# Kernel tuning notes

Hardware: AMD Instinct MI355X
Metric: run time of the kernel (lower is better)

The kernel has to match this reference:

```python
import jax, jax.numpy as jnp
import numpy as np

N_NODES = 1024      # nNodes
N_EDGES = 4096      # nEdges
N_FACTORS = 64      # input feature dim (rows of kernel / paths)
BATCH = 256
NNZ_PER_ROW = 32    # nonzeros per kernel row -> iter = count_nonzero = 32 exactly
N_SOURCES = 16


def setup_inputs() -> dict:
    key = jax.random.key(0)
    k1, k2 = jax.random.split(key, 2)
    x = jax.random.normal(k1, (BATCH, N_FACTORS), dtype=jnp.float32)

    rng = np.random.default_rng(0)
    lin = rng.choice(N_NODES * N_NODES, size=N_EDGES, replace=False)
    # Edges[e] = (col, row): original scatters node_prop[i, Edges[e][1], Edges[e][0]] = paths[i][e]
    edges = np.stack([lin % N_NODES, lin // N_NODES], axis=1).astype(np.int64)

    sources = np.sort(rng.choice(N_NODES, size=N_SOURCES, replace=False)).astype(np.int64)

    # kernel ("paths") with exactly NNZ_PER_ROW nonzeros per row, so the
    # data-dependent propagation depth count_nonzero(paths[i]) == NNZ_PER_ROW
    cols = np.argsort(rng.random((N_FACTORS, N_EDGES)), axis=1)[:, :NNZ_PER_ROW]
    mask = np.zeros((N_FACTORS, N_EDGES), dtype=np.float32)
    mask[np.arange(N_FACTORS)[:, None], cols] = 1.0
    dense = np.asarray(jax.random.normal(k2, (N_FACTORS, N_EDGES), dtype=jnp.float32)) * 0.1
    kernel = jnp.asarray(dense * mask)

    return {
        "x": x,
        "kernel": kernel,
        "edges": jnp.asarray(edges),
        "sources": jnp.asarray(sources),
    }


def reference(x, kernel, edges, sources):
    F, E = kernel.shape
    N = N_NODES

    # scatter-build per-factor adjacency: node_prop[i, dst, src] = kernel[i, e]
    node_prop = jnp.zeros((F, N, N), x.dtype).at[:, edges[:, 1], edges[:, 0]].set(kernel)
    # row 0 fixed so each column sums to 1
    node_prop = node_prop.at[:, 0, :].set(1.0 - node_prop.sum(axis=1))

    source_flow = jnp.zeros((N,), x.dtype).at[sources].set(1.0)

    # data-dependent propagation depth per factor
    iters = jnp.count_nonzero(kernel, axis=1)  # [F], == NNZ_PER_ROW by construction

    # prop_flow[i] is linear in factor[i]; propagate the unit source vector per factor
    V0 = jnp.broadcast_to(source_flow, (F, N))

    def step(V, t):
        Vn = jnp.einsum('fij,fj->fi', node_prop, V)
        return jnp.where(t < iters[:, None], Vn, V), None

    V, _ = jax.lax.scan(step, V0, jnp.arange(NNZ_PER_ROW))

    # subtract factor[i] at every source node: W[i] = V[i] - 1_{sources}
    W = V - source_flow  # [F, N]

    prop_flows = x @ W        # [B, N]  (sum over factors of scaled propagated flows)
    recon = x @ kernel        # [B, E]  linear-combination reconstruction
    return prop_flows, recon
```

## Files before the change

### kernel.cpp

```cpp
#include <hip/hip_runtime.h>
#include <hip/hip_bf16.h>

#define NNODES   1024
#define NEDGES   4096
#define NFACT    64
#define NBATCH   256
#define NSRC     16
#define MAXNNZ   64
#define MAXITER  32

__global__ __launch_bounds__(64) void prop_kernel(
    const float* __restrict__ kern,
    const int*   __restrict__ edges,
    const int*   __restrict__ sources,
    float*       __restrict__ W)
{
    __shared__ float v_lds[NNODES];
    __shared__ float wbuf[MAXNNZ];
    __shared__ int   srcbuf[MAXNNZ];
    __shared__ int   dstbuf[MAXNNZ];
    __shared__ float c_lds[MAXNNZ];
    __shared__ int   cnt;

    const int f = blockIdx.x;
    const int t = threadIdx.x;

    if (t == 0) cnt = 0;
    __syncthreads();

    const float4* kern4 = (const float4*)kern;
    for (int i = 0; i < NEDGES / 4 / 64; ++i) {
        int e4 = t + i * 64;
        float4 kv = kern4[f * (NEDGES / 4) + e4];
        float vals[4] = {kv.x, kv.y, kv.z, kv.w};
        #pragma unroll
        for (int c = 0; c < 4; ++c) {
            if (vals[c] != 0.0f) {
                int e = e4 * 4 + c;
                int slot = atomicAdd(&cnt, 1);
                if (slot < MAXNNZ) {
                    wbuf[slot]   = vals[c];
                    srcbuf[slot] = edges[e * 2 + 0];
                    dstbuf[slot] = edges[e * 2 + 1];
                }
            }
        }
    }
    __syncthreads();

    int nnz = cnt;
    if (nnz > MAXNNZ) nnz = MAXNNZ;
    const int T = nnz < MAXITER ? nnz : MAXITER;

    const bool active = (t < nnz);
    const float w_e  = active ? wbuf[t]   : 0.0f;
    const int   src  = active ? srcbuf[t] : -1;
    const int   dst  = active ? dstbuf[t] : -1;

    unsigned long long gmask = 0ull;
    for (int e2 = 0; e2 < nnz; ++e2) {
        if (dstbuf[e2] == src) gmask |= (1ull << e2);
    }

    float S = (float)NSRC;
    float val = 0.0f;
    #pragma unroll
    for (int s = 0; s < NSRC; ++s) {
        if (sources[s] == src) val = 1.0f;
    }

    float c_last = 0.0f, v0_last = 0.0f;

    for (int it = 0; it < T; ++it) {
        float c = w_e * val;
        c_lds[t] = c;

        float a = c;
        float b = (dst == 0) ? c : 0.0f;
        #pragma unroll
        for (int o = 16; o >= 1; o >>= 1) {
            a += __shfl_xor(a, o);
            b += __shfl_xor(b, o);
        }
        float C = a, C0 = b;

        float v0 = S - C;
        S = S - C0;

        float nv = 0.0f;
        unsigned long long m = gmask;
        while (m) {
            int i = __ffsll(m) - 1;
            nv += c_lds[i];
            m &= m - 1;
        }
        val = (src == 0) ? v0 : nv;

        c_last = c; v0_last = v0;
    }

    for (int n = t; n < NNODES; n += 64) v_lds[n] = 0.0f;
    __syncthreads();
    if (T > 0) {
        if (t == 0) v_lds[0] = v0_last;
        if (active && dst != 0) atomicAdd(&v_lds[dst], c_last);
    } else {
        if (t < NSRC) v_lds[sources[t]] = 1.0f;
    }
    __syncthreads();
    if (t < NSRC) atomicAdd(&v_lds[sources[t]], -1.0f);
    __syncthreads();

    float4* Wrow4 = (float4*)(W + f * NNODES);
    const float4* v4 = (const float4*)v_lds;
    #pragma unroll
    for (int i = 0; i < NNODES / 4 / 64; ++i)
        Wrow4[t + i * 64] = v4[t + i * 64];
}

__global__ __launch_bounds__(256) void out_kernel(
    const float* __restrict__ x,
    const float* __restrict__ W,
    const float* __restrict__ kern,
    float*       __restrict__ out)
{
    const int NP4 = NBATCH * NNODES / 4;
    const int NR4 = NBATCH * NEDGES / 4;
    int idx = blockIdx.x * blockDim.x + threadIdx.x;
    float4* out4 = (float4*)out;

    if (idx < NP4) {
        int b  = idx >> 8;
        int n4 = idx & 255;
        const float4* Wv = (const float4*)W;
        float4 acc = {0.f, 0.f, 0.f, 0.f};
        #pragma unroll
        for (int k = 0; k < NFACT; ++k) {
            float xv = x[b * NFACT + k];
            float4 wv = Wv[k * 256 + n4];
            acc.x += xv * wv.x; acc.y += xv * wv.y;
            acc.z += xv * wv.z; acc.w += xv * wv.w;
        }
        out4[idx] = acc;
    } else if (idx < NP4 + NR4) {
        int j  = idx - NP4;
        int b  = j >> 10;
        int e4 = j & 1023;
        const float4* Kv = (const float4*)kern;
        float4 acc = {0.f, 0.f, 0.f, 0.f};
        #pragma unroll
        for (int k = 0; k < NFACT; ++k) {
            float xv = x[b * NFACT + k];
            float4 kv = Kv[k * 1024 + e4];
            acc.x += xv * kv.x; acc.y += xv * kv.y;
            acc.z += xv * kv.z; acc.w += xv * kv.w;
        }
        out4[NP4 + j] = acc;
    }
}

extern "C" void kernel_launch(void* const* d_in, const int* in_sizes, int n_in,
                              void* d_out, int out_size, void* d_ws, size_t ws_size,
                              hipStream_t stream) {
    const float* x       = (const float*)d_in[0];
    const float* kern    = (const float*)d_in[1];
    const int*   edges   = (const int*)d_in[2];
    const int*   sources = (const int*)d_in[3];
    float* out = (float*)d_out;
    float* W   = (float*)d_ws;

    prop_kernel<<<NFACT, 64, 0, stream>>>(kern, edges, sources, W);

    const int total4 = NBATCH * NNODES / 4 + NBATCH * NEDGES / 4;
    out_kernel<<<(total4 + 255) / 256, 256, 0, stream>>>(x, W, kern, out);
}
```

Baseline: 96.80 us.

## Overlap recon GEMM with propagation and add fast path for chain-graph propagation

Moves the x@kernel reconstruction into the propagation launch as extra blocks, so it runs concurrently with the 64 serial per-factor propagation blocks instead of after them. Propagation blocks grow to 256 threads for the loads, and a fast path is added: when no edge touches node 0 and each edge has at most one predecessor, the per-iteration LDS gather and two reductions become a single shuffle. Both GEMM-like kernels now compute two batch rows per thread to reuse each weight load. The old general path is kept as a fallback, and the wave reductions now span 64 lanes instead of 32.

```diff
diff --git a/kernel.cpp b/kernel.cpp
--- a/kernel.cpp
+++ b/kernel.cpp
@@ -9,12 +9,38 @@
 #define MAXNNZ   64
 #define MAXITER  32
 
-__global__ __launch_bounds__(64) void prop_kernel(
+#define RECON_BLOCKS 512
+#define FLOWS_BLOCKS 128
+
+__global__ __launch_bounds__(256) void k1(
     const float* __restrict__ kern,
     const int*   __restrict__ edges,
     const int*   __restrict__ sources,
-    float*       __restrict__ W)
+    const float* __restrict__ x,
+    float*       __restrict__ W,
+    float*       __restrict__ out)
 {
+    if (blockIdx.x >= NFACT) {
+        int r  = blockIdx.x - NFACT;
+        int e4 = (r & 3) * 256 + threadIdx.x;
+        int b0 = (r >> 2) * 2;
+        const float4* Kv  = (const float4*)kern;
+        const float*  xr0 = x + b0 * NFACT;
+        const float*  xr1 = xr0 + NFACT;
+        float4 a0 = {0.f,0.f,0.f,0.f}, a1 = {0.f,0.f,0.f,0.f};
+        #pragma unroll 4
+        for (int k = 0; k < NFACT; ++k) {
+            float4 kv = Kv[k * (NEDGES/4) + e4];
+            float x0 = xr0[k], x1 = xr1[k];
+            a0.x += x0*kv.x; a0.y += x0*kv.y; a0.z += x0*kv.z; a0.w += x0*kv.w;
+            a1.x += x1*kv.x; a1.y += x1*kv.y; a1.z += x1*kv.z; a1.w += x1*kv.w;
+        }
+        float4* o4 = (float4*)(out + NBATCH * NNODES);
+        o4[ b0      * (NEDGES/4) + e4] = a0;
+        o4[(b0 + 1) * (NEDGES/4) + e4] = a1;
+        return;
+    }
+
     __shared__ float v_lds[NNODES];
     __shared__ float wbuf[MAXNNZ];
     __shared__ int   srcbuf[MAXNNZ];
@@ -28,135 +54,124 @@
     if (t == 0) cnt = 0;
     __syncthreads();
 
-    const float4* kern4 = (const float4*)kern;
-    for (int i = 0; i < NEDGES / 4 / 64; ++i) {
-        int e4 = t + i * 64;
-        float4 kv = kern4[f * (NEDGES / 4) + e4];
+    const float4* kern4 = (const float4*)(kern + f * NEDGES);
+    #pragma unroll
+    for (int i = 0; i < NEDGES/4/256; ++i) {
+        int e4 = t + i * 256;
+        float4 kv = kern4[e4];
         float vals[4] = {kv.x, kv.y, kv.z, kv.w};
         #pragma unroll
         for (int c = 0; c < 4; ++c) {
-            if (vals[c] != 0.0f) {
-                int e = e4 * 4 + c;
+            if (vals[c] != 0.f) {
                 int slot = atomicAdd(&cnt, 1);
                 if (slot < MAXNNZ) {
                     wbuf[slot]   = vals[c];
-                    srcbuf[slot] = edges[e * 2 + 0];
-                    dstbuf[slot] = edges[e * 2 + 1];
+                    int e        = e4 * 4 + c;
+                    srcbuf[slot] = edges[2*e];
+                    dstbuf[slot] = edges[2*e + 1];
                 }
             }
         }
     }
     __syncthreads();
 
-    int nnz = cnt;
-    if (nnz > MAXNNZ) nnz = MAXNNZ;
-    const int T = nnz < MAXITER ? nnz : MAXITER;
+    const int nnz = min(cnt, MAXNNZ);
+    const int T   = min(nnz, MAXITER);
 
-    const bool active = (t < nnz);
-    const float w_e  = active ? wbuf[t]   : 0.0f;
-    const int   src  = active ? srcbuf[t] : -1;
-    const int   dst  = active ? dstbuf[t] : -1;
+    for (int n = t; n < NNODES; n += 256) v_lds[n] = 0.f;
+    __syncthreads();
 
-    unsigned long long gmask = 0ull;
-    for (int e2 = 0; e2 < nnz; ++e2) {
-        if (dstbuf[e2] == src) gmask |= (1ull << e2);
-    }
+    if (t < 64) {
+        const bool  active = (t < nnz);
+        const float w_e = active ? wbuf[t]   : 0.f;
+        const int   src = active ? srcbuf[t] : -1;
+        const int   dst = active ? dstbuf[t] : -1;
 
-    float S = (float)NSRC;
-    float val = 0.0f;
-    #pragma unroll
-    for (int s = 0; s < NSRC; ++s) {
-        if (sources[s] == src) val = 1.0f;
-    }
+        unsigned long long gmask = 0ull;
+        for (int e2 = 0; e2 < nnz; ++e2)
+            if (dstbuf[e2] == src) gmask |= (1ull << e2);
 
-    float c_last = 0.0f, v0_last = 0.0f;
+        float val = 0.f;
+        for (int s = 0; s < NSRC; ++s)
+            if (sources[s] == src) val = 1.f;
+        float S = (float)NSRC;
 
-    for (int it = 0; it < T; ++it) {
-        float c = w_e * val;
-        c_lds[t] = c;
+        unsigned long long anybad =
+            __ballot(active && (src == 0 || dst == 0)) |
+            __ballot(__popcll(gmask) > 1);
 
-        float a = c;
-        float b = (dst == 0) ? c : 0.0f;
-        #pragma unroll
-        for (int o = 16; o >= 1; o >>= 1) {
-            a += __shfl_xor(a, o);
-            b += __shfl_xor(b, o);
+        if (T > 0) {
+            float c_fin = 0.f, v0_fin = 0.f;
+            if (anybad == 0ull) {
+                const int   gidx = gmask ? (__ffsll(gmask) - 1) : t;
+                const float gsel = gmask ? 1.f : 0.f;
+                float c = 0.f;
+                for (int it = 0; it < T; ++it) {
+                    c = w_e * val;
+                    float g = __shfl(c, gidx);
+                    val = gsel * g;
+                }
+                float a = c;
+                #pragma unroll
+                for (int o = 32; o >= 1; o >>= 1) a += __shfl_xor(a, o);
+                c_fin = c; v0_fin = S - a;
+            } else {
+                float c = 0.f, v0 = 0.f;
+                for (int it = 0; it < T; ++it) {
+                    c = w_e * val;
+                    c_lds[t] = c;
+                    float a = c;
+                    float b = (dst == 0) ? c : 0.f;
+                    #pragma unroll
+                    for (int o = 32; o >= 1; o >>= 1) {
+                        a += __shfl_xor(a, o);
+                        b += __shfl_xor(b, o);
+                    }
+                    v0 = S - a;
+                    S  = S - b;
+                    float nv = 0.f;
+                    unsigned long long m = gmask;
+                    while (m) { int i = __ffsll(m) - 1; nv += c_lds[i]; m &= m - 1; }
+                    val = (src == 0) ? v0 : nv;
+                }
+                c_fin = c; v0_fin = v0;
+            }
+            if (t == 0) v_lds[0] = v0_fin;
+            if (active && dst != 0) atomicAdd(&v_lds[dst], c_fin);
+        } else {
+            if (t < NSRC) v_lds[sources[t]] = 1.f;
         }
-        float C = a, C0 = b;
-
-        float v0 = S - C;
-        S = S - C0;
-
-        float nv = 0.0f;
-        unsigned long long m = gmask;
-        while (m) {
-            int i = __ffsll(m) - 1;
-            nv += c_lds[i];
-            m &= m - 1;
-        }
-        val = (src == 0) ? v0 : nv;
-
-        c_last = c; v0_last = v0;
-    }
-
-    for (int n = t; n < NNODES; n += 64) v_lds[n] = 0.0f;
-    __syncthreads();
-    if (T > 0) {
-        if (t == 0) v_lds[0] = v0_last;
-        if (active && dst != 0) atomicAdd(&v_lds[dst], c_last);
-    } else {
-        if (t < NSRC) v_lds[sources[t]] = 1.0f;
     }
     __syncthreads();
-    if (t < NSRC) atomicAdd(&v_lds[sources[t]], -1.0f);
+    if (t < NSRC) atomicAdd(&v_lds[sources[t]], -1.f);
     __syncthreads();
 
-    float4* Wrow4 = (float4*)(W + f * NNODES);
+    float4* Wr = (float4*)(W + f * NNODES);
     const float4* v4 = (const float4*)v_lds;
-    #pragma unroll
-    for (int i = 0; i < NNODES / 4 / 64; ++i)
-        Wrow4[t + i * 64] = v4[t + i * 64];
+    Wr[t] = v4[t];
 }
 
-__global__ __launch_bounds__(256) void out_kernel(
+__global__ __launch_bounds__(256) void k2(
     const float* __restrict__ x,
     const float* __restrict__ W,
-    const float* __restrict__ kern,
     float*       __restrict__ out)
 {
-    const int NP4 = NBATCH * NNODES / 4;
-    const int NR4 = NBATCH * NEDGES / 4;
-    int idx = blockIdx.x * blockDim.x + threadIdx.x;
-    float4* out4 = (float4*)out;
-
-    if (idx < NP4) {
-        int b  = idx >> 8;
-        int n4 = idx & 255;
-        const float4* Wv = (const float4*)W;
-        float4 acc = {0.f, 0.f, 0.f, 0.f};
-        #pragma unroll
-        for (int k = 0; k < NFACT; ++k) {
-            float xv = x[b * NFACT + k];
-            float4 wv = Wv[k * 256 + n4];
-            acc.x += xv * wv.x; acc.y += xv * wv.y;
-            acc.z += xv * wv.z; acc.w += xv * wv.w;
-        }
-        out4[idx] = acc;
-    } else if (idx < NP4 + NR4) {
-        int j  = idx - NP4;
-        int b  = j >> 10;
-        int e4 = j & 1023;
-        const float4* Kv = (const float4*)kern;
-        float4 acc = {0.f, 0.f, 0.f, 0.f};
-        #pragma unroll
-        for (int k = 0; k < NFACT; ++k) {
-            float xv = x[b * NFACT + k];
-            float4 kv = Kv[k * 1024 + e4];
-            acc.x += xv * kv.x; acc.y += xv * kv.y;
-            acc.z += xv * kv.z; acc.w += xv * kv.w;
-        }
-        out4[NP4 + j] = acc;
+    const int b0 = blockIdx.x * 2;
+    const int t  = threadIdx.x;
+    const float4* Wv  = (const float4*)W;
+    const float*  xr0 = x + b0 * NFACT;
+    const float*  xr1 = xr0 + NFACT;
+    float4 a0 = {0.f,0.f,0.f,0.f}, a1 = {0.f,0.f,0.f,0.f};
+    #pragma unroll 4
+    for (int k = 0; k < NFACT; ++k) {
+        float4 wv = Wv[k * (NNODES/4) + t];
+        float x0 = xr0[k], x1 = xr1[k];
+        a0.x += x0*wv.x; a0.y += x0*wv.y; a0.z += x0*wv.z; a0.w += x0*wv.w;
+        a1.x += x1*wv.x; a1.y += x1*wv.y; a1.z += x1*wv.z; a1.w += x1*wv.w;
     }
+    float4* o4 = (float4*)out;
+    o4[ b0      * (NNODES/4) + t] = a0;
+    o4[(b0 + 1) * (NNODES/4) + t] = a1;
 }
 
 extern "C" void kernel_launch(void* const* d_in, const int* in_sizes, int n_in,
@@ -169,8 +184,6 @@
     float* out = (float*)d_out;
     float* W   = (float*)d_ws;
 
-    prop_kernel<<<NFACT, 64, 0, stream>>>(kern, edges, sources, W);
-
-    const int total4 = NBATCH * NNODES / 4 + NBATCH * NEDGES / 4;
-    out_kernel<<<(total4 + 255) / 256, 256, 0, stream>>>(x, W, kern, out);
+    k1<<<NFACT + RECON_BLOCKS, 256, 0, stream>>>(kern, edges, sources, x, W, out);
+    k2<<<FLOWS_BLOCKS, 256, 0, stream>>>(x, W, out);
 }
```

New measurement: 83.11 us. -14.1%, faster.
